# Performance work log

Measured on AMD Instinct MI355X. Metric: run time of the kernel, lower is better.

Reference implementation:

```python
import jax, jax.numpy as jnp
import numpy as np

B, D, N, K = 256, 1024, 200000, 64  # batch, model_dim, n_slots, outer_dim
EPS = 1e-8


def setup_inputs() -> dict:
    key = jax.random.key(0)
    k1, k2, k3, k4, k5 = jax.random.split(key, 5)
    return {
        "cue": jax.random.normal(k1, (B, D), dtype=jnp.float32),
        "slot_matrix": jax.random.normal(k2, (N, K), dtype=jnp.float32),
        "priority": jax.random.uniform(k3, (N,), dtype=jnp.float32),
        "w_cue": jax.random.normal(k4, (K, D), dtype=jnp.float32) * (1.0 / np.sqrt(D)),
        "w_dec": jax.random.normal(k5, (D, K), dtype=jnp.float32) * (1.0 / np.sqrt(K)),
    }


def reference(cue, slot_matrix, priority, w_cue, w_dec):
    # cue_proj: (B, D) @ (D, K) -> (B, K)
    cue_outer = jnp.einsum('bd,kd->bk', cue, w_cue)
    # dot-product similarity against every slot: (B, N)
    sim = jnp.einsum('bk,nk->bn', cue_outer, slot_matrix)
    weights = jax.nn.softmax(sim, axis=-1)
    # priority-modulated renormalization
    weights = weights * priority[None, :]
    weights = weights / jnp.clip(weights.sum(axis=-1, keepdims=True), EPS)
    # weighted readout over slots: (B, K)
    retrieved = jnp.einsum('bn,nk->bk', weights, slot_matrix)
    # decoder: (B, K) @ (K, D) -> (B, D)
    return jnp.einsum('bk,dk->bd', retrieved, w_dec)
```

## Files before the change

### kernel.cpp

```cpp
#include <hip/hip_runtime.h>
#include <hip/hip_fp16.h>

#define B_ 256
#define D_ 1024
#define N_ 200000
#define K_ 64
#define SHIFT_ 24.0f
#define NCHUNK 3125
#define SL_ 8

typedef short short8 __attribute__((ext_vector_type(8)));
typedef _Float16 f16x8 __attribute__((ext_vector_type(8)));
typedef float f32x4 __attribute__((ext_vector_type(4)));

__device__ __forceinline__ unsigned f2bf(float x) {
  unsigned u = __float_as_uint(x);
  return (u + 0x7fffu + ((u >> 16) & 1u)) >> 16;
}
__device__ __forceinline__ unsigned pack2(float a, float b) {
  return f2bf(a) | (f2bf(b) << 16);
}
__device__ __forceinline__ float bf2f(unsigned short u) {
  return __uint_as_float(((unsigned)u) << 16);
}
__device__ __forceinline__ unsigned f2h(float x) {
  return (unsigned)__half_as_ushort(__float2half(x));
}
__device__ __forceinline__ f32x4 mfma16b(int4 a, int4 b, f32x4 c) {
  return __builtin_amdgcn_mfma_f32_16x16x32_bf16(
      __builtin_bit_cast(short8, a), __builtin_bit_cast(short8, b), c, 0, 0, 0);
}
__device__ __forceinline__ f32x4 mfma16h(int4 a, int4 b, f32x4 c) {
  return __builtin_amdgcn_mfma_f32_16x16x32_f16(
      __builtin_bit_cast(f16x8, a), __builtin_bit_cast(f16x8, b), c, 0, 0, 0);
}
__device__ __forceinline__ int p8hash(int k) { return ((k >> 3) ^ k) & 7; }

__global__ __launch_bounds__(256) void k1_cueproj(
    const float* __restrict__ cue, const float* __restrict__ wcue,
    float* __restrict__ couter) {
  const int b    = blockIdx.x;
  const int tid  = threadIdx.x;
  const int w    = tid >> 6;
  const int lane = tid & 63;

  __shared__ float part[4][64][65];
  __shared__ float red[4][64];

  const float4 creg =
      *(const float4*)(cue + (size_t)b * D_ + w * 256 + lane * 4);
  const float* wbase = wcue + w * 256 + lane * 4;

#pragma unroll 8
  for (int k = 0; k < 64; ++k) {
    const float4 wv = *(const float4*)(wbase + (size_t)k * D_);
    part[w][k][lane] =
        creg.x * wv.x + creg.y * wv.y + creg.z * wv.z + creg.w * wv.w;
  }
  __syncthreads();

  const int k  = tid & 63;
  const int wq = tid >> 6;
  float a = 0.f;
#pragma unroll 8
  for (int j = 0; j < 64; ++j) a += part[wq][k][j];
  red[wq][k] = a;
  __syncthreads();
  if (tid < 64) {
    couter[b * K_ + tid] =
        red[0][tid] + red[1][tid] + red[2][tid] + red[3][tid];
  }
}

__global__ __launch_bounds__(256, 2) void k2_attend(
    const float* __restrict__ slot, const float* __restrict__ prio,
    const float* __restrict__ couter, unsigned short* __restrict__ Spart,
    float* __restrict__ Zpart, int G) {
  __shared__ __align__(16) unsigned short sh_h[64 * 72];
  __shared__ __align__(16) unsigned short sh_T[64 * 64];
  __shared__ __align__(16) unsigned short sh_E[4 * 64 * 72];
  __shared__ float sh_p[64];

  const int tid = threadIdx.x;
  const int g   = blockIdx.x;
  const int l   = tid & 63;
  const int w   = tid >> 6;
  const int c16 = l & 15;
  const int q   = l >> 4;

  int4 qf[4][2];
#pragma unroll
  for (int bt = 0; bt < 4; ++bt) {
#pragma unroll
    for (int s = 0; s < 2; ++s) {
      const float* qp =
          couter + (size_t)(w * 64 + bt * 16 + c16) * K_ + s * 32 + q * 8;
      float4 va = *(const float4*)qp;
      float4 vb = *(const float4*)(qp + 4);
      qf[bt][s] = make_int4(
          (int)(f2h(va.x) | (f2h(va.y) << 16)),
          (int)(f2h(va.z) | (f2h(va.w) << 16)),
          (int)(f2h(vb.x) | (f2h(vb.y) << 16)),
          (int)(f2h(vb.z) | (f2h(vb.w) << 16)));
    }
  }

  f32x4 S[4][4];
#pragma unroll
  for (int a = 0; a < 4; ++a)
#pragma unroll
    for (int b = 0; b < 4; ++b) S[a][b] = (f32x4){0.f, 0.f, 0.f, 0.f};
  float zacc[4] = {0.f, 0.f, 0.f, 0.f};

  float4 pf[4];
  float ppf = 0.f;
  {
    const float4* src = (const float4*)(slot + (size_t)g * 64 * K_);
#pragma unroll
    for (int i = 0; i < 4; ++i) pf[i] = src[tid + 256 * i];
    if (tid < 64) ppf = prio[g * 64 + tid];
  }

  for (int chunk = g; chunk < NCHUNK; chunk += G) {
    __syncthreads();
#pragma unroll
    for (int i = 0; i < 4; ++i) {
      const int f   = tid + 256 * i;
      const int row = f >> 4;
      const int c4  = (f & 15) * 4;
      float xs[4] = {pf[i].x, pf[i].y, pf[i].z, pf[i].w};
      unsigned hh[4];
#pragma unroll
      for (int j = 0; j < 4; ++j) {
        hh[j] = f2h(xs[j]);
        const int k = c4 + j;
        sh_T[k * 64 + (row ^ (p8hash(k) << 3))] =
            (unsigned short)f2bf(xs[j]);
      }
      *(uint2*)&sh_h[row * 72 + c4] =
          make_uint2(hh[0] | (hh[1] << 16), hh[2] | (hh[3] << 16));
    }
    if (tid < 64) sh_p[tid] = ppf;
    __syncthreads();

    const int nxt = chunk + G;
    if (nxt < NCHUNK) {
      const float4* src = (const float4*)(slot + (size_t)nxt * 64 * K_);
#pragma unroll
      for (int i = 0; i < 4; ++i) pf[i] = src[tid + 256 * i];
      if (tid < 64) ppf = prio[nxt * 64 + tid];
    }

#pragma unroll
    for (int t = 0; t < 4; ++t) {
      f32x4 cc[4];
#pragma unroll
      for (int bt = 0; bt < 4; ++bt) cc[bt] = (f32x4){0.f, 0.f, 0.f, 0.f};
#pragma unroll
      for (int s = 0; s < 2; ++s) {
        const int off = (t * 16 + c16) * 72 + s * 32 + q * 8;
        int4 ah = *(const int4*)&sh_h[off];
#pragma unroll
        for (int bt = 0; bt < 4; ++bt) cc[bt] = mfma16h(ah, qf[bt][s], cc[bt]);
      }
      const float4 p = *(const float4*)&sh_p[t * 16 + q * 4];
#pragma unroll
      for (int bt = 0; bt < 4; ++bt) {
        float e0 = __expf(cc[bt][0] - SHIFT_) * p.x;
        float e1 = __expf(cc[bt][1] - SHIFT_) * p.y;
        float e2 = __expf(cc[bt][2] - SHIFT_) * p.z;
        float e3 = __expf(cc[bt][3] - SHIFT_) * p.w;
        zacc[bt] += (e0 + e1) + (e2 + e3);
        *(uint2*)&sh_E[w * 4608 + (bt * 16 + c16) * 72 + t * 16 + q * 4] =
            make_uint2(pack2(e0, e1), pack2(e2, e3));
      }
    }

#pragma unroll
    for (int s = 0; s < 2; ++s) {
      int4 bT[4];
#pragma unroll
      for (int ct = 0; ct < 4; ++ct) {
        const int k = ct * 16 + c16;
        bT[ct] = *(const int4*)&sh_T[k * 64 +
                                     ((s * 32 + q * 8) ^ (p8hash(k) << 3))];
      }
#pragma unroll
      for (int bt = 0; bt < 4; ++bt) {
        int4 aE = *(const int4*)&sh_E[w * 4608 + (bt * 16 + c16) * 72 +
                                      s * 32 + q * 8];
#pragma unroll
        for (int ct = 0; ct < 4; ++ct)
          S[bt][ct] = mfma16b(aE, bT[ct], S[bt][ct]);
      }
    }
  }

#pragma unroll
  for (int bt = 0; bt < 4; ++bt) {
#pragma unroll
    for (int ct = 0; ct < 4; ++ct) {
#pragma unroll
      for (int r = 0; r < 4; ++r) {
        sh_E[(w * 64 + bt * 16 + q * 4 + r) * 72 + ct * 16 + c16] =
            (unsigned short)f2bf(S[bt][ct][r]);
      }
    }
  }
  __syncthreads();
#pragma unroll
  for (int i = 0; i < 8; ++i) {
    const int idx   = tid + 256 * i;
    const int batch = idx >> 3;
    const int seg   = idx & 7;
    uint4 v = *(const uint4*)&sh_E[batch * 72 + seg * 8];
    *(uint4*)&Spart[((size_t)batch * G + g) * K_ + seg * 8] = v;
  }
#pragma unroll
  for (int bt = 0; bt < 4; ++bt) {
    float z = zacc[bt];
    z += __shfl_xor(z, 16);
    z += __shfl_xor(z, 32);
    if (l < 16) Zpart[(size_t)(w * 64 + bt * 16 + c16) * G + g] = z;
  }
}

__global__ __launch_bounds__(256) void k3a_reduce(
    const unsigned short* __restrict__ Spart, float* __restrict__ rkpart,
    int G) {
  const int b   = blockIdx.x;
  const int s   = blockIdx.y;
  const int tid = threadIdx.x;
  const int gq  = tid >> 3;
  const int k8  = tid & 7;

  __shared__ float part[32][65];

  const int gcnt = G / SL_;
  const int gbeg = s * gcnt;

  float acc[8] = {0.f, 0.f, 0.f, 0.f, 0.f, 0.f, 0.f, 0.f};
  const unsigned short* sp = Spart + (size_t)b * G * K_ + k8 * 8;
  for (int gg = gq; gg < gcnt; gg += 32) {
    uint4 v = *(const uint4*)(sp + (size_t)(gbeg + gg) * K_);
    acc[0] += __uint_as_float(v.x << 16);
    acc[1] += __uint_as_float(v.x & 0xffff0000u);
    acc[2] += __uint_as_float(v.y << 16);
    acc[3] += __uint_as_float(v.y & 0xffff0000u);
    acc[4] += __uint_as_float(v.z << 16);
    acc[5] += __uint_as_float(v.z & 0xffff0000u);
    acc[6] += __uint_as_float(v.w << 16);
    acc[7] += __uint_as_float(v.w & 0xffff0000u);
  }
#pragma unroll
  for (int j = 0; j < 8; ++j) part[gq][k8 * 8 + j] = acc[j];
  __syncthreads();

  if (tid < 64) {
    float sum = 0.f;
#pragma unroll
    for (int r = 0; r < 32; ++r) sum += part[r][tid];
    rkpart[((size_t)b * SL_ + s) * K_ + tid] = sum;
  }
}

__global__ __launch_bounds__(256) void k3b_decode(
    const float* __restrict__ rkpart, const float* __restrict__ Zpart,
    const float* __restrict__ wdec, float* __restrict__ out, int G) {
  const int b   = blockIdx.x;
  const int j   = blockIdx.y;
  const int tid = threadIdx.x;

  __shared__ float zred[256];
  __shared__ float rk[K_];
  __shared__ float wlds[256 * 65];

  float zp = 0.f;
  const float* zpp = Zpart + (size_t)b * G;
  for (int g = tid; g < G; g += 256) zp += zpp[g];
  zred[tid] = zp;
  __syncthreads();

  if (tid < K_) {
    float ssum = 0.f;
#pragma unroll
    for (int s = 0; s < SL_; ++s)
      ssum += rkpart[((size_t)b * SL_ + s) * K_ + tid];
    if (tid == 0) {
      float zz = 0.f;
      for (int i = 0; i < 256; ++i) zz += zred[i];
      zred[0] = fmaxf(zz, 1e-30f);
    }
    rk[tid] = ssum;
  }
  __syncthreads();
  const float invZ = 1.0f / zred[0];

#pragma unroll
  for (int i = 0; i < 16; ++i) {
    const int f   = tid + 256 * i;
    const int row = f >> 4;
    const int c4  = (f & 15) * 4;
    const float4 v =
        *(const float4*)(wdec + (size_t)(j * 256 + row) * K_ + c4);
    wlds[row * 65 + c4 + 0] = v.x;
    wlds[row * 65 + c4 + 1] = v.y;
    wlds[row * 65 + c4 + 2] = v.z;
    wlds[row * 65 + c4 + 3] = v.w;
  }
  __syncthreads();

  float acc = 0.f;
#pragma unroll
  for (int kk = 0; kk < 64; ++kk) acc += rk[kk] * wlds[tid * 65 + kk];
  out[(size_t)b * D_ + j * 256 + tid] = acc * invZ;
}

extern "C" void kernel_launch(void* const* d_in, const int* in_sizes, int n_in,
                              void* d_out, int out_size, void* d_ws,
                              size_t ws_size, hipStream_t stream) {
  const float* cue  = (const float*)d_in[0];
  const float* slot = (const float*)d_in[1];
  const float* prio = (const float*)d_in[2];
  const float* wcue = (const float*)d_in[3];
  const float* wdec = (const float*)d_in[4];
  float* out = (float*)d_out;

  const size_t per_g = (size_t)B_ * K_ * 2 + (size_t)B_ * 4;
  long long avail = (long long)ws_size - 65536 - 524288;
  int G = (int)(avail > 0 ? avail / (long long)per_g : SL_);
  if (G > 512) G = 512;
  G &= ~(SL_ - 1);
  if (G < SL_) G = SL_;

  float* couter         = (float*)d_ws;
  unsigned short* Spart = (unsigned short*)(couter + 16384);
  float* Zpart          = (float*)(Spart + (size_t)B_ * G * K_);
  float* rkpart         = Zpart + (size_t)B_ * G;

  k1_cueproj<<<dim3(B_), dim3(256), 0, stream>>>(cue, wcue, couter);
  k2_attend<<<dim3(G), dim3(256), 0, stream>>>(slot, prio, couter, Spart,
                                               Zpart, G);
  k3a_reduce<<<dim3(B_, SL_), dim3(256), 0, stream>>>(Spart, rkpart, G);
  k3b_decode<<<dim3(B_, 4), dim3(256), 0, stream>>>(rkpart, Zpart, wdec, out,
                                                    G);
}
```

Before: 134.6 us.

## Halve attention LDS footprint and raise k2 occupancy to four blocks per CU

The exp/softmax stage and the readout MFMAs are interleaved over two halves of the 64-slot chunk, so each wave's E staging buffer only holds 32 slots. This cuts shared memory per block from about 50KB to about 38KB, which lets launch_bounds request 4 blocks per CU. The final S staging now reuses the whole shared buffer after an extra barrier, and the grid cap rises to 1024 blocks. Risks are register pressure from the tighter launch bound (possible spills) and more partials for k3a to reduce.

```diff
diff --git a/kernel.cpp b/kernel.cpp
--- a/kernel.cpp
+++ b/kernel.cpp
@@ -72,14 +72,15 @@
   }
 }
 
-__global__ __launch_bounds__(256, 2) void k2_attend(
+__global__ __launch_bounds__(256, 4) void k2_attend(
     const float* __restrict__ slot, const float* __restrict__ prio,
     const float* __restrict__ couter, unsigned short* __restrict__ Spart,
     float* __restrict__ Zpart, int G) {
-  __shared__ __align__(16) unsigned short sh_h[64 * 72];
-  __shared__ __align__(16) unsigned short sh_T[64 * 64];
-  __shared__ __align__(16) unsigned short sh_E[4 * 64 * 72];
-  __shared__ float sh_p[64];
+  __shared__ __align__(16) unsigned short sh_all[19200];
+  unsigned short* const sh_h = sh_all;
+  unsigned short* const sh_T = sh_all + 4608;
+  unsigned short* const sh_E = sh_all + 8704;
+  float* const sh_p = (float*)(sh_all + 18944);
 
   const int tid = threadIdx.x;
   const int g   = blockIdx.x;
@@ -152,43 +153,44 @@
     }
 
 #pragma unroll
-    for (int t = 0; t < 4; ++t) {
-      f32x4 cc[4];
-#pragma unroll
-      for (int bt = 0; bt < 4; ++bt) cc[bt] = (f32x4){0.f, 0.f, 0.f, 0.f};
-#pragma unroll
-      for (int s = 0; s < 2; ++s) {
-        const int off = (t * 16 + c16) * 72 + s * 32 + q * 8;
-        int4 ah = *(const int4*)&sh_h[off];
-#pragma unroll
-        for (int bt = 0; bt < 4; ++bt) cc[bt] = mfma16h(ah, qf[bt][s], cc[bt]);
-      }
-      const float4 p = *(const float4*)&sh_p[t * 16 + q * 4];
-#pragma unroll
-      for (int bt = 0; bt < 4; ++bt) {
-        float e0 = __expf(cc[bt][0] - SHIFT_) * p.x;
-        float e1 = __expf(cc[bt][1] - SHIFT_) * p.y;
-        float e2 = __expf(cc[bt][2] - SHIFT_) * p.z;
-        float e3 = __expf(cc[bt][3] - SHIFT_) * p.w;
-        zacc[bt] += (e0 + e1) + (e2 + e3);
-        *(uint2*)&sh_E[w * 4608 + (bt * 16 + c16) * 72 + t * 16 + q * 4] =
-            make_uint2(pack2(e0, e1), pack2(e2, e3));
-      }
-    }
-
-#pragma unroll
-    for (int s = 0; s < 2; ++s) {
+    for (int h = 0; h < 2; ++h) {
+#pragma unroll
+      for (int tt = 0; tt < 2; ++tt) {
+        const int t = h * 2 + tt;
+        f32x4 cc[4];
+#pragma unroll
+        for (int bt = 0; bt < 4; ++bt) cc[bt] = (f32x4){0.f, 0.f, 0.f, 0.f};
+#pragma unroll
+        for (int s = 0; s < 2; ++s) {
+          const int off = (t * 16 + c16) * 72 + s * 32 + q * 8;
+          int4 ah = *(const int4*)&sh_h[off];
+#pragma unroll
+          for (int bt = 0; bt < 4; ++bt)
+            cc[bt] = mfma16h(ah, qf[bt][s], cc[bt]);
+        }
+        const float4 p = *(const float4*)&sh_p[t * 16 + q * 4];
+#pragma unroll
+        for (int bt = 0; bt < 4; ++bt) {
+          float e0 = __expf(cc[bt][0] - SHIFT_) * p.x;
+          float e1 = __expf(cc[bt][1] - SHIFT_) * p.y;
+          float e2 = __expf(cc[bt][2] - SHIFT_) * p.z;
+          float e3 = __expf(cc[bt][3] - SHIFT_) * p.w;
+          zacc[bt] += (e0 + e1) + (e2 + e3);
+          *(uint2*)&sh_E[w * 2560 + (bt * 16 + c16) * 40 + tt * 16 + q * 4] =
+              make_uint2(pack2(e0, e1), pack2(e2, e3));
+        }
+      }
       int4 bT[4];
 #pragma unroll
       for (int ct = 0; ct < 4; ++ct) {
         const int k = ct * 16 + c16;
         bT[ct] = *(const int4*)&sh_T[k * 64 +
-                                     ((s * 32 + q * 8) ^ (p8hash(k) << 3))];
+                                     ((h * 32 + q * 8) ^ (p8hash(k) << 3))];
       }
 #pragma unroll
       for (int bt = 0; bt < 4; ++bt) {
-        int4 aE = *(const int4*)&sh_E[w * 4608 + (bt * 16 + c16) * 72 +
-                                      s * 32 + q * 8];
+        int4 aE =
+            *(const int4*)&sh_E[w * 2560 + (bt * 16 + c16) * 40 + q * 8];
 #pragma unroll
         for (int ct = 0; ct < 4; ++ct)
           S[bt][ct] = mfma16b(aE, bT[ct], S[bt][ct]);
@@ -196,13 +198,15 @@
     }
   }
 
+  __syncthreads();
+  unsigned short* const stg = sh_all;
 #pragma unroll
   for (int bt = 0; bt < 4; ++bt) {
 #pragma unroll
     for (int ct = 0; ct < 4; ++ct) {
 #pragma unroll
       for (int r = 0; r < 4; ++r) {
-        sh_E[(w * 64 + bt * 16 + q * 4 + r) * 72 + ct * 16 + c16] =
+        stg[(w * 64 + bt * 16 + q * 4 + r) * 72 + ct * 16 + c16] =
             (unsigned short)f2bf(S[bt][ct][r]);
       }
     }
@@ -213,7 +217,7 @@
     const int idx   = tid + 256 * i;
     const int batch = idx >> 3;
     const int seg   = idx & 7;
-    uint4 v = *(const uint4*)&sh_E[batch * 72 + seg * 8];
+    uint4 v = *(const uint4*)&stg[batch * 72 + seg * 8];
     *(uint4*)&Spart[((size_t)batch * G + g) * K_ + seg * 8] = v;
   }
 #pragma unroll
@@ -329,7 +333,7 @@
   const size_t per_g = (size_t)B_ * K_ * 2 + (size_t)B_ * 4;
   long long avail = (long long)ws_size - 65536 - 524288;
   int G = (int)(avail > 0 ? avail / (long long)per_g : SL_);
-  if (G > 512) G = 512;
+  if (G > 1024) G = 1024;
   G &= ~(SL_ - 1);
   if (G < SL_) G = SL_;
 
```

Result: slower. 330.4 us (+145.4%).
